# Kernel tuning notes

Hardware: AMD Instinct MI355X
Metric: run time of the kernel (lower is better)

Reference implementation:

```python
import jax, jax.numpy as jnp
import numpy as np

N_NODES = 100000
N_RELS = 8
N_EDGES = 150000
D_IN = 128
D_OUT = 128


def setup_inputs() -> dict:
    key = jax.random.key(0)
    k1, k2, k3, k4, k5 = jax.random.split(key, 5)
    scale = 1.0 / np.sqrt(D_IN)
    return {
        "x": jax.random.normal(k1, (N_NODES, D_IN), dtype=jnp.float32),
        "weight": jax.random.normal(k2, (N_RELS, D_IN, D_OUT), dtype=jnp.float32) * scale,
        "self_loop_weight": jax.random.normal(k3, (D_IN, D_OUT), dtype=jnp.float32) * scale,
        "bias": jnp.zeros((D_OUT,), dtype=jnp.float32),
        "src": jax.random.randint(k4, (N_RELS, N_EDGES), 0, N_NODES, dtype=jnp.int64),
        "dst": jax.random.randint(k5, (N_RELS, N_EDGES), 0, N_NODES, dtype=jnp.int64),
    }


def reference(x, weight, self_loop_weight, bias, src, dst):
    # Per-relation GraphConv(norm='right'): for each dst node, mean of incoming
    # src features (sum / in-degree, degree clamped to 1), then matmul W_r.
    # HeteroGraphConv sums relation outputs; then self-loop, bias, relu.
    n = x.shape[0]

    def per_rel(s, d, W):
        msgs = jax.ops.segment_sum(x[s], d, num_segments=n)          # [N, D_IN]
        deg = jax.ops.segment_sum(jnp.ones_like(s, dtype=x.dtype), d,
                                  num_segments=n)                     # [N]
        msgs = msgs / jnp.maximum(deg, 1.0)[:, None]
        return msgs @ W                                               # [N, D_OUT]

    agg = jax.vmap(per_rel)(src, dst, weight).sum(axis=0)             # [N, D_OUT]
    out = agg + x @ self_loop_weight + bias
    return jax.nn.relu(out)
```

## Files before the change

### kernel.cpp

```cpp
#include <hip/hip_runtime.h>
#include <hip/hip_bf16.h>
#include <stdint.h>

#define N_NODES 100000
#define N_RELS  8
#define N_EDGES 150000
#define KCOLS   1152
#define CAP     64

#define EB_BLOCKS   587
#define EDGE_SECT   (EB_BLOCKS * N_RELS)
#define CAST_BLOCKS 6250
#define PREP_BLOCKS 576
#define TOTAL_PRE   (EDGE_SECT + CAST_BLOCKS + PREP_BLOCKS)

typedef short bf16x8 __attribute__((ext_vector_type(8)));
typedef float f32x4  __attribute__((ext_vector_type(4)));
typedef unsigned int u32;

__device__ __forceinline__ unsigned short f2b(float f) {
    union { float f; unsigned u; } v; v.f = f;
    unsigned r = v.u + 0x7FFF + ((v.u >> 16) & 1);
    return (unsigned short)(r >> 16);
}

__device__ __forceinline__ void gld16(const void* g, void* lds_uniform) {
    __builtin_amdgcn_global_load_lds(
        (const __attribute__((address_space(1))) u32*)g,
        (__attribute__((address_space(3))) u32*)lds_uniform,
        16, 0, 0);
}


__global__ __launch_bounds__(256) void fused_pre(
    const float* __restrict__ x, const float* __restrict__ W,
    const float* __restrict__ Wself,
    const int* __restrict__ src, const int* __restrict__ dst,
    unsigned short* __restrict__ xb, unsigned short* __restrict__ BT2,
    int* __restrict__ cnt, int* __restrict__ ebuf) {
    int b = blockIdx.x;
    int tid = threadIdx.x;
    if (b < EDGE_SECT) {
        int r = b / EB_BLOCKS, eb = b - r * EB_BLOCKS;
        int e = eb * 256 + tid;
        if (e < N_EDGES) {
            int s = src[r * N_EDGES + e];
            int d = dst[r * N_EDGES + e];
            int slot = atomicAdd(&cnt[d], 1);
            if (slot < CAP) ebuf[d * CAP + slot] = (r << 17) | s;
        }
    } else if (b < EDGE_SECT + CAST_BLOCKS) {
        int t = (b - EDGE_SECT) * 256 + tid;
        if (t < N_NODES * 16) {
            int row = t >> 4, g = t & 15;
            const float4* p = (const float4*)(x + (size_t)row * 128 + g * 8);
            float4 a = p[0], bb = p[1];
            unsigned short o[8] = { f2b(a.x), f2b(a.y), f2b(a.z), f2b(a.w),
                                    f2b(bb.x), f2b(bb.y), f2b(bb.z), f2b(bb.w) };
            int g2 = (g & 8) | ((g & 7) ^ (row & 7));
            *(int4*)(xb + (size_t)row * 128 + (g2 << 3)) = *(const int4*)o;
        }
    } else {
        int flat = (b - EDGE_SECT - CAST_BLOCKS) * 256 + tid;
        if (flat < 128 * KCOLS) {
            int n = flat / KCOLS, k = flat - n * KCOLS;
            float v;
            if (k < 1024) {
                int r = k >> 7, kk = k & 127;
                v = W[(r << 14) + (kk << 7) + n];
            } else {
                v = Wself[((k - 1024) << 7) + n];
            }
            int t2 = k >> 6, kb = (k >> 5) & 1, quad = (k >> 3) & 3, e = k & 7;
            int wc = n >> 6, j = (n >> 4) & 3, ml = n & 15;
            size_t idx = ((((((size_t)t2 * 2 + kb) * 2 + wc) * 4 + j) * 4 + quad)
                          << 7) + (ml << 3) + e;
            BT2[idx] = f2b(v);
        }
    }
}

__global__ __launch_bounds__(256) void agg_x(
    const unsigned short* __restrict__ xb, const int* __restrict__ ebuf,
    const int* __restrict__ cnt, unsigned short* __restrict__ Agg) {
    int d = (blockIdx.x << 2) + (threadIdx.x >> 6);
    if (d >= N_NODES) return;
    d = __builtin_amdgcn_readfirstlane(d);
    int lane = threadIdx.x & 63;

    int k = cnt[d]; if (k > CAP) k = CAP;
    k = __builtin_amdgcn_readfirstlane(k);
    int rec = (lane < k) ? ebuf[d * CAP + lane] : -1;
    int rl = rec >> 17;

    const unsigned int* xw = (const unsigned int*)xb;

    unsigned long long mask[8];
#pragma unroll
    for (int r = 0; r < 8; ++r) mask[r] = __ballot(rl == r);

    unsigned long long below = (lane == 63) ? 0x7FFFFFFFFFFFFFFFull
                                            : ((1ull << lane) - 1);
    int pre = 0;
    unsigned long long mymask = 0;
#pragma unroll
    for (int r = 0; r < 8; ++r) {
        pre += (rl > r) ? (int)__popcll(mask[r]) : 0;
        mymask = (rl == r) ? mask[r] : mymask;
    }
    int pos = (rl >= 0) ? (pre + (int)__popcll(mymask & below)) : lane;
    int srt = __builtin_amdgcn_ds_permute(pos << 2, rec);

    int swu = lane ^ ((d & 7) << 2);
    unsigned int* aggRow = (unsigned int*)(Agg + (size_t)d * 1024);

    auto store_r = [&](int rconst, float ax, float ay, int dg) {
        float inv = 1.0f / (float)(dg < 1 ? 1 : dg);
        unsigned int pk = (unsigned int)f2b(ax * inv)
                        | ((unsigned int)f2b(ay * inv) << 16);
        aggRow[(rconst << 6) + swu] = pk;
    };
    auto flush = [&](int r, float ax, float ay) {
        switch (r) {
            case 0: store_r(0, ax, ay, (int)__popcll(mask[0])); break;
            case 1: store_r(1, ax, ay, (int)__popcll(mask[1])); break;
            case 2: store_r(2, ax, ay, (int)__popcll(mask[2])); break;
            case 3: store_r(3, ax, ay, (int)__popcll(mask[3])); break;
            case 4: store_r(4, ax, ay, (int)__popcll(mask[4])); break;
            case 5: store_r(5, ax, ay, (int)__popcll(mask[5])); break;
            case 6: store_r(6, ax, ay, (int)__popcll(mask[6])); break;
            default: store_r(7, ax, ay, (int)__popcll(mask[7])); break;
        }
    };

    float axc = 0.f, ayc = 0.f;
    int cur = 0;
    if (k > 0) cur = __builtin_amdgcn_readlane(srt, 0) >> 17;

    for (int i = 0; i < k; i += 4) {
        int rc4[4];
#pragma unroll
        for (int j = 0; j < 4; ++j) {
            int ii = i + j; if (ii > k - 1) ii = k - 1;
            rc4[j] = __builtin_amdgcn_readlane(srt, ii);
        }
        unsigned int y4[4];
#pragma unroll
        for (int j = 0; j < 4; ++j) {
            int s = rc4[j] & 0x1FFFF;
            y4[j] = xw[(size_t)s * 64 + (lane ^ ((s & 7) << 2))];
        }
#pragma unroll
        for (int j = 0; j < 4; ++j) {
            if (i + j < k) {
                int rr = rc4[j] >> 17;
                if (rr != cur) {
                    flush(cur, axc, ayc);
                    axc = 0.f; ayc = 0.f; cur = rr;
                }
                union { unsigned u; float f; } vx, vy;
                vx.u = y4[j] << 16;
                vy.u = y4[j] & 0xFFFF0000u;
                axc += vx.f;
                ayc += vy.f;
            }
        }
    }
    if (k > 0) flush(cur, axc, ayc);

#pragma unroll
    for (int r = 0; r < 8; ++r)
        if (mask[r] == 0) aggRow[(r << 6) + swu] = 0u;
}

__global__ __launch_bounds__(256, 4) void gemm_out(
    const unsigned short* __restrict__ Agg, const unsigned short* __restrict__ xb,
    const unsigned short* __restrict__ BT2, const float* __restrict__ bias,
    float* __restrict__ out) {
    __shared__ short As[2][128 * 64];
    int t = threadIdx.x;
    int rowBase = blockIdx.x * 128;

    int w = t >> 6, lane = t & 63;
    int wr = w >> 1, wc = w & 1;
    int ml = lane & 15, quad = lane >> 4;
    int sa = (lane & 7) << 4;

    int ri = lane >> 3;
    int cb = (lane & 7) << 4;

    f32x4 acc[4][4];
#pragma unroll
    for (int i = 0; i < 4; ++i)
#pragma unroll
        for (int j = 0; j < 4; ++j)
            acc[i][j] = (f32x4){0.f, 0.f, 0.f, 0.f};

    auto stage = [&](int buf, int t2) {
        int kc = t2 >> 1, h = t2 & 1;
#pragma unroll
        for (int j = 0; j < 4; ++j) {
            int i = (w << 2) + j;
            int row = (i << 3) + ri;
            int grow = rowBase + row;
            if (grow > N_NODES - 1) grow = N_NODES - 1;
            const char* ga = (kc < 8)
                ? (const char*)Agg + (size_t)grow * 2048 + (kc << 8) + (h << 7) + cb
                : (const char*)xb  + (size_t)grow * 256  + (h << 7) + cb;
            gld16(ga, (char*)&As[buf][0] + (i << 10));
        }
    };

    auto compute = [&](int buf, int t2) {
#pragma unroll
        for (int kb = 0; kb < 2; ++kb) {
            int off = ((kb << 6) + (quad << 4)) ^ sa;
            bf16x8 a[4], b[4];
#pragma unroll
            for (int i = 0; i < 4; ++i)
                a[i] = *(const bf16x8*)((const char*)&As[buf][0] +
                        (((wr << 6) + (i << 4) + ml) << 7) + off);
#pragma unroll
            for (int j = 0; j < 4; ++j) {
                size_t fb = (((((size_t)(t2 << 1) + kb) * 2 + wc) * 4 + j) << 9)
                          + ((size_t)lane << 3);
                b[j] = *(const bf16x8*)&BT2[fb];
            }
#pragma unroll
            for (int i = 0; i < 4; ++i)
#pragma unroll
                for (int j = 0; j < 4; ++j)
                    acc[i][j] = __builtin_amdgcn_mfma_f32_16x16x32_bf16(a[i], b[j], acc[i][j], 0, 0, 0);
        }
    };

    stage(0, 0);
    asm volatile("s_waitcnt vmcnt(0)" ::: "memory");
    __syncthreads();
    int cur = 0;
    for (int t2 = 0; t2 < 18; ++t2) {
        if (t2 + 1 < 18) stage(cur ^ 1, t2 + 1);
        compute(cur, t2);
        asm volatile("s_waitcnt vmcnt(0)" ::: "memory");
        __syncthreads();
        cur ^= 1;
    }

#pragma unroll
    for (int i = 0; i < 4; ++i) {
#pragma unroll
        for (int j = 0; j < 4; ++j) {
            int col = wc * 64 + j * 16 + ml;
            float bv = bias[col];
#pragma unroll
            for (int rr = 0; rr < 4; ++rr) {
                int row = rowBase + wr * 64 + i * 16 + quad * 4 + rr;
                if (row < N_NODES) {
                    float v = acc[i][j][rr] + bv;
                    out[(size_t)row * 128 + col] = fmaxf(v, 0.f);
                }
            }
        }
    }
}

extern "C" void kernel_launch(void* const* d_in, const int* in_sizes, int n_in,
                              void* d_out, int out_size, void* d_ws, size_t ws_size,
                              hipStream_t stream) {
    const float* x     = (const float*)d_in[0];
    const float* W     = (const float*)d_in[1];
    const float* Wself = (const float*)d_in[2];
    const float* bias  = (const float*)d_in[3];
    const int*   src   = (const int*)d_in[4];
    const int*   dst   = (const int*)d_in[5];
    float* out = (float*)d_out;

    char* ws = (char*)d_ws;
    size_t off = 0;
    unsigned short* Agg = (unsigned short*)(ws + off); off += (size_t)N_NODES * 1024 * 2;
    unsigned short* xb  = (unsigned short*)(ws + off); off += (size_t)N_NODES * 128 * 2;
    unsigned short* BT2 = (unsigned short*)(ws + off); off += (size_t)128 * KCOLS * 2;
    int* cnt  = (int*)(ws + off); off += (size_t)N_NODES * 4;
    int* ebuf = (int*)(ws + off); off += (size_t)N_NODES * CAP * 4;

    hipMemsetAsync(cnt, 0, (size_t)N_NODES * 4, stream);

    fused_pre<<<TOTAL_PRE, 256, 0, stream>>>(x, W, Wself, src, dst,
                                             xb, BT2, cnt, ebuf);

    agg_x<<<(N_NODES + 3) / 4, 256, 0, stream>>>(xb, ebuf, cnt, Agg);

    gemm_out<<<(N_NODES + 127) / 128, 256, 0, stream>>>(Agg, xb, BT2, bias, out);
}
```

Before: 319.9 us.

## Reorder to transform-then-aggregate: per-relation GEMM into Z, then gather-mean into output

Swaps the order of aggregation and projection. A new GEMM computes x·W_r for all eight relations plus the self-loop into a bf16 buffer Z, and writes the biased self-loop result straight to out. The aggregation kernel then gathers projected rows from Z per edge, scales them by the inverse degree, and adds them to out before applying relu. This removes the zero-fill of the Agg buffer and the long K=1152 GEMM loop. In exchange, the edge gathers now hit a 200 MB Z table instead of the small bf16 x, and out is read back and written a second time.

```diff
diff --git a/kernel.cpp b/kernel.cpp
--- a/kernel.cpp
+++ b/kernel.cpp
@@ -36,7 +36,7 @@
     const float* __restrict__ x, const float* __restrict__ W,
     const float* __restrict__ Wself,
     const int* __restrict__ src, const int* __restrict__ dst,
-    unsigned short* __restrict__ xb, unsigned short* __restrict__ BT2,
+    unsigned short* __restrict__ xb, unsigned short* __restrict__ W2,
     int* __restrict__ cnt, int* __restrict__ ebuf) {
     int b = blockIdx.x;
     int tid = threadIdx.x;
@@ -64,25 +64,129 @@
         int flat = (b - EDGE_SECT - CAST_BLOCKS) * 256 + tid;
         if (flat < 128 * KCOLS) {
             int n = flat / KCOLS, k = flat - n * KCOLS;
-            float v;
-            if (k < 1024) {
-                int r = k >> 7, kk = k & 127;
-                v = W[(r << 14) + (kk << 7) + n];
-            } else {
-                v = Wself[((k - 1024) << 7) + n];
+            int c = k >> 7, kw = k & 127;
+            float v = (c < 8) ? W[(c << 14) + (kw << 7) + n]
+                              : Wself[(kw << 7) + n];
+            int t2 = kw >> 6, kb = (kw >> 5) & 1, quad = (kw >> 3) & 3,
+                e = kw & 7;
+            int wc = n >> 6, jj = (n >> 4) & 3, mll = n & 15;
+            size_t idx = (size_t)((((c * 2 + t2) * 2 + kb) * 2 + wc) * 4 + jj)
+                         * 512 + (((quad << 4) + mll) << 3) + e;
+            W2[idx] = f2b(v);
+        }
+    }
+}
+
+__global__ __launch_bounds__(256, 4) void gemm_z(
+    const unsigned short* __restrict__ xb, const unsigned short* __restrict__ W2,
+    const float* __restrict__ bias, unsigned short* __restrict__ Z,
+    float* __restrict__ out) {
+    __shared__ short As[2][128 * 64];
+    int t = threadIdx.x;
+    int bid = blockIdx.x;
+    int rb = bid / 9, c = bid - rb * 9;
+    int rowBase = rb * 128;
+
+    int w = t >> 6, lane = t & 63;
+    int wr = w >> 1, wc = w & 1;
+    int ml = lane & 15, quad = lane >> 4;
+    int sa = (lane & 7) << 4;
+    int ri = lane >> 3;
+    int cb = (lane & 7) << 4;
+
+    f32x4 acc[4][4];
+#pragma unroll
+    for (int i = 0; i < 4; ++i)
+#pragma unroll
+        for (int j = 0; j < 4; ++j)
+            acc[i][j] = (f32x4){0.f, 0.f, 0.f, 0.f};
+
+    auto stage = [&](int buf, int t2) {
+#pragma unroll
+        for (int j = 0; j < 4; ++j) {
+            int i = (w << 2) + j;
+            int row = (i << 3) + ri;
+            int grow = rowBase + row;
+            if (grow > N_NODES - 1) grow = N_NODES - 1;
+            const char* ga = (const char*)xb + (size_t)grow * 256
+                           + (t2 << 7) + cb;
+            gld16(ga, (char*)&As[buf][0] + (i << 10));
+        }
+    };
+
+    auto compute = [&](int buf, int t2) {
+#pragma unroll
+        for (int kb = 0; kb < 2; ++kb) {
+            int off = ((kb << 6) + (quad << 4)) ^ sa;
+            bf16x8 a[4], b[4];
+#pragma unroll
+            for (int i = 0; i < 4; ++i)
+                a[i] = *(const bf16x8*)((const char*)&As[buf][0] +
+                        (((wr << 6) + (i << 4) + ml) << 7) + off);
+#pragma unroll
+            for (int j = 0; j < 4; ++j) {
+                size_t fb = (size_t)((((c * 2 + t2) * 2 + kb) * 2 + wc) * 4 + j)
+                            * 512 + ((size_t)lane << 3);
+                b[j] = *(const bf16x8*)&W2[fb];
             }
-            int t2 = k >> 6, kb = (k >> 5) & 1, quad = (k >> 3) & 3, e = k & 7;
-            int wc = n >> 6, j = (n >> 4) & 3, ml = n & 15;
-            size_t idx = ((((((size_t)t2 * 2 + kb) * 2 + wc) * 4 + j) * 4 + quad)
-                          << 7) + (ml << 3) + e;
-            BT2[idx] = f2b(v);
+#pragma unroll
+            for (int i = 0; i < 4; ++i)
+#pragma unroll
+                for (int j = 0; j < 4; ++j)
+                    acc[i][j] = __builtin_amdgcn_mfma_f32_16x16x32_bf16(a[i], b[j], acc[i][j], 0, 0, 0);
+        }
+    };
+
+    stage(0, 0);
+    asm volatile("s_waitcnt vmcnt(0)" ::: "memory");
+    __syncthreads();
+    stage(1, 1);
+    compute(0, 0);
+    asm volatile("s_waitcnt vmcnt(0)" ::: "memory");
+    __syncthreads();
+    compute(1, 1);
+
+    if (c < 8) {
+#pragma unroll
+        for (int i = 0; i < 4; ++i) {
+#pragma unroll
+            for (int j = 0; j < 4; ++j) {
+#pragma unroll
+                for (int rr = 0; rr < 4; ++rr) {
+                    float v = acc[i][j][rr];
+                    float o = __shfl_xor(v, 1);
+                    if ((lane & 1) == 0) {
+                        unsigned int pk = (unsigned int)f2b(v)
+                                        | ((unsigned int)f2b(o) << 16);
+                        int row = rowBase + wr * 64 + i * 16 + quad * 4 + rr;
+                        int col = wc * 64 + j * 16 + ml;
+                        if (row < N_NODES)
+                            *(unsigned int*)&Z[(size_t)row * 1024 + (c << 7) + col] = pk;
+                    }
+                }
+            }
+        }
+    } else {
+#pragma unroll
+        for (int i = 0; i < 4; ++i) {
+#pragma unroll
+            for (int j = 0; j < 4; ++j) {
+                int col = wc * 64 + j * 16 + ml;
+                float bv = bias[col];
+#pragma unroll
+                for (int rr = 0; rr < 4; ++rr) {
+                    int row = rowBase + wr * 64 + i * 16 + quad * 4 + rr;
+                    if (row < N_NODES)
+                        out[(size_t)row * 128 + col] = acc[i][j][rr] + bv;
+                }
+            }
         }
     }
 }
 
-__global__ __launch_bounds__(256) void agg_x(
-    const unsigned short* __restrict__ xb, const int* __restrict__ ebuf,
-    const int* __restrict__ cnt, unsigned short* __restrict__ Agg) {
+__global__ __launch_bounds__(256) void agg_out(
+    const unsigned short* __restrict__ Z, const int* __restrict__ ebuf,
+    const int* __restrict__ cnt, float* __restrict__ out) {
     int d = (blockIdx.x << 2) + (threadIdx.x >> 6);
     if (d >= N_NODES) return;
     d = __builtin_amdgcn_readfirstlane(d);
@@ -93,7 +197,7 @@
     int rec = (lane < k) ? ebuf[d * CAP + lane] : -1;
     int rl = rec >> 17;
 
-    const unsigned int* xw = (const unsigned int*)xb;
+    const unsigned int* Zu = (const unsigned int*)Z;
 
     unsigned long long mask[8];
 #pragma unroll
@@ -111,26 +215,23 @@
     int pos = (rl >= 0) ? (pre + (int)__popcll(mymask & below)) : lane;
     int srt = __builtin_amdgcn_ds_permute(pos << 2, rec);
 
-    int swu = lane ^ ((d & 7) << 2);
-    unsigned int* aggRow = (unsigned int*)(Agg + (size_t)d * 1024);
-
-    auto store_r = [&](int rconst, float ax, float ay, int dg) {
+    float ox = 0.f, oy = 0.f;
+
+    auto flush = [&](int r, float ax, float ay) {
+        int dg;
+        switch (r) {
+            case 0: dg = (int)__popcll(mask[0]); break;
+            case 1: dg = (int)__popcll(mask[1]); break;
+            case 2: dg = (int)__popcll(mask[2]); break;
+            case 3: dg = (int)__popcll(mask[3]); break;
+            case 4: dg = (int)__popcll(mask[4]); break;
+            case 5: dg = (int)__popcll(mask[5]); break;
+            case 6: dg = (int)__popcll(mask[6]); break;
+            default: dg = (int)__popcll(mask[7]); break;
+        }
         float inv = 1.0f / (float)(dg < 1 ? 1 : dg);
-        unsigned int pk = (unsigned int)f2b(ax * inv)
-                        | ((unsigned int)f2b(ay * inv) << 16);
-        aggRow[(rconst << 6) + swu] = pk;
-    };
-    auto flush = [&](int r, float ax, float ay) {
-        switch (r) {
-            case 0: store_r(0, ax, ay, (int)__popcll(mask[0])); break;
-            case 1: store_r(1, ax, ay, (int)__popcll(mask[1])); break;
-            case 2: store_r(2, ax, ay, (int)__popcll(mask[2])); break;
-            case 3: store_r(3, ax, ay, (int)__popcll(mask[3])); break;
-            case 4: store_r(4, ax, ay, (int)__popcll(mask[4])); break;
-            case 5: store_r(5, ax, ay, (int)__popcll(mask[5])); break;
-            case 6: store_r(6, ax, ay, (int)__popcll(mask[6])); break;
-            default: store_r(7, ax, ay, (int)__popcll(mask[7])); break;
-        }
+        ox += ax * inv;
+        oy += ay * inv;
     };
 
     float axc = 0.f, ayc = 0.f;
@@ -148,7 +249,8 @@
 #pragma unroll
         for (int j = 0; j < 4; ++j) {
             int s = rc4[j] & 0x1FFFF;
-            y4[j] = xw[(size_t)s * 64 + (lane ^ ((s & 7) << 2))];
+            int r = rc4[j] >> 17;
+            y4[j] = Zu[(size_t)s * 512 + (r << 6) + lane];
         }
 #pragma unroll
         for (int j = 0; j < 4; ++j) {
@@ -168,100 +270,11 @@
     }
     if (k > 0) flush(cur, axc, ayc);
 
-#pragma unroll
-    for (int r = 0; r < 8; ++r)
-        if (mask[r] == 0) aggRow[(r << 6) + swu] = 0u;
-}
-
-__global__ __launch_bounds__(256, 4) void gemm_out(
-    const unsigned short* __restrict__ Agg, const unsigned short* __restrict__ xb,
-    const unsigned short* __restrict__ BT2, const float* __restrict__ bias,
-    float* __restrict__ out) {
-    __shared__ short As[2][128 * 64];
-    int t = threadIdx.x;
-    int rowBase = blockIdx.x * 128;
-
-    int w = t >> 6, lane = t & 63;
-    int wr = w >> 1, wc = w & 1;
-    int ml = lane & 15, quad = lane >> 4;
-    int sa = (lane & 7) << 4;
-
-    int ri = lane >> 3;
-    int cb = (lane & 7) << 4;
-
-    f32x4 acc[4][4];
-#pragma unroll
-    for (int i = 0; i < 4; ++i)
-#pragma unroll
-        for (int j = 0; j < 4; ++j)
-            acc[i][j] = (f32x4){0.f, 0.f, 0.f, 0.f};
-
-    auto stage = [&](int buf, int t2) {
-        int kc = t2 >> 1, h = t2 & 1;
-#pragma unroll
-        for (int j = 0; j < 4; ++j) {
-            int i = (w << 2) + j;
-            int row = (i << 3) + ri;
-            int grow = rowBase + row;
-            if (grow > N_NODES - 1) grow = N_NODES - 1;
-            const char* ga = (kc < 8)
-                ? (const char*)Agg + (size_t)grow * 2048 + (kc << 8) + (h << 7) + cb
-                : (const char*)xb  + (size_t)grow * 256  + (h << 7) + cb;
-            gld16(ga, (char*)&As[buf][0] + (i << 10));
-        }
-    };
-
-    auto compute = [&](int buf, int t2) {
-#pragma unroll
-        for (int kb = 0; kb < 2; ++kb) {
-            int off = ((kb << 6) + (quad << 4)) ^ sa;
-            bf16x8 a[4], b[4];
-#pragma unroll
-            for (int i = 0; i < 4; ++i)
-                a[i] = *(const bf16x8*)((const char*)&As[buf][0] +
-                        (((wr << 6) + (i << 4) + ml) << 7) + off);
-#pragma unroll
-            for (int j = 0; j < 4; ++j) {
-                size_t fb = (((((size_t)(t2 << 1) + kb) * 2 + wc) * 4 + j) << 9)
-                          + ((size_t)lane << 3);
-                b[j] = *(const bf16x8*)&BT2[fb];
-            }
-#pragma unroll
-            for (int i = 0; i < 4; ++i)
-#pragma unroll
-                for (int j = 0; j < 4; ++j)
-                    acc[i][j] = __builtin_amdgcn_mfma_f32_16x16x32_bf16(a[i], b[j], acc[i][j], 0, 0, 0);
-        }
-    };
-
-    stage(0, 0);
-    asm volatile("s_waitcnt vmcnt(0)" ::: "memory");
-    __syncthreads();
-    int cur = 0;
-    for (int t2 = 0; t2 < 18; ++t2) {
-        if (t2 + 1 < 18) stage(cur ^ 1, t2 + 1);
-        compute(cur, t2);
-        asm volatile("s_waitcnt vmcnt(0)" ::: "memory");
-        __syncthreads();
-        cur ^= 1;
-    }
-
-#pragma unroll
-    for (int i = 0; i < 4; ++i) {
-#pragma unroll
-        for (int j = 0; j < 4; ++j) {
-            int col = wc * 64 + j * 16 + ml;
-            float bv = bias[col];
-#pragma unroll
-            for (int rr = 0; rr < 4; ++rr) {
-                int row = rowBase + wr * 64 + i * 16 + quad * 4 + rr;
-                if (row < N_NODES) {
-                    float v = acc[i][j][rr] + bv;
-                    out[(size_t)row * 128 + col] = fmaxf(v, 0.f);
-                }
-            }
-        }
-    }
+    float2 prev = *(const float2*)&out[(size_t)d * 128 + (lane << 1)];
+    float2 res;
+    res.x = fmaxf(ox + prev.x, 0.f);
+    res.y = fmaxf(oy + prev.y, 0.f);
+    *(float2*)&out[(size_t)d * 128 + (lane << 1)] = res;
 }
 
 extern "C" void kernel_launch(void* const* d_in, const int* in_sizes, int n_in,
@@ -277,18 +290,18 @@
 
     char* ws = (char*)d_ws;
     size_t off = 0;
-    unsigned short* Agg = (unsigned short*)(ws + off); off += (size_t)N_NODES * 1024 * 2;
-    unsigned short* xb  = (unsigned short*)(ws + off); off += (size_t)N_NODES * 128 * 2;
-    unsigned short* BT2 = (unsigned short*)(ws + off); off += (size_t)128 * KCOLS * 2;
+    unsigned short* Z  = (unsigned short*)(ws + off); off += (size_t)N_NODES * 1024 * 2;
+    unsigned short* xb = (unsigned short*)(ws + off); off += (size_t)N_NODES * 128 * 2;
+    unsigned short* W2 = (unsigned short*)(ws + off); off += (size_t)128 * KCOLS * 2;
     int* cnt  = (int*)(ws + off); off += (size_t)N_NODES * 4;
     int* ebuf = (int*)(ws + off); off += (size_t)N_NODES * CAP * 4;
 
     hipMemsetAsync(cnt, 0, (size_t)N_NODES * 4, stream);
 
     fused_pre<<<TOTAL_PRE, 256, 0, stream>>>(x, W, Wself, src, dst,
-                                             xb, BT2, cnt, ebuf);
-
-    agg_x<<<(N_NODES + 3) / 4, 256, 0, stream>>>(xb, ebuf, cnt, Agg);
-
-    gemm_out<<<(N_NODES + 127) / 128, 256, 0, stream>>>(Agg, xb, BT2, bias, out);
-}
+                                             xb, W2, cnt, ebuf);
+
+    gemm_z<<<((N_NODES + 127) / 128) * 9, 256, 0, stream>>>(xb, W2, bias, Z, out);
+
+    agg_out<<<(N_NODES + 3) / 4, 256, 0, stream>>>(Z, ebuf, cnt, out);
+}
```

Result: slower. 359.3 us (+12.3%).
